# Performance work log

Measured on AMD Instinct MI355X. Metric: run time of the kernel, lower is better.

Reference implementation:

```python
import jax, jax.numpy as jnp
import numpy as np

B, N, C, H = 1, 128, 128, 8
D = C // H
SCALE = D ** -0.5


def layer_norm(x, w, b, eps=1e-5):
    m = jnp.mean(x, axis=-1, keepdims=True)
    v = jnp.var(x, axis=-1, keepdims=True)
    return (x - m) * jax.lax.rsqrt(v + eps) * w + b


def setup_inputs() -> dict:
    key = jax.random.key(0)
    ks = jax.random.split(key, 8)
    s = 0.02
    return {
        "e": jax.random.normal(ks[0], (B, N, N, C), jnp.float32),
        "mask": jnp.zeros((B, N, N, 1), jnp.float32),
        "ln_w": jnp.ones((C,), jnp.float32),
        "ln_b": jnp.zeros((C,), jnp.float32),
        "w_qkv_in": jax.random.normal(ks[1], (C, 3 * C), jnp.float32) * s,
        "b_qkv_in": jnp.zeros((3 * C,), jnp.float32),
        "w_eg_in": jax.random.normal(ks[2], (C, 2 * H), jnp.float32) * s,
        "b_eg_in": jnp.zeros((2 * H,), jnp.float32),
        "w_qkv_out": jax.random.normal(ks[3], (C, 3 * C), jnp.float32) * s,
        "b_qkv_out": jnp.zeros((3 * C,), jnp.float32),
        "w_eg_out": jax.random.normal(ks[4], (C, 2 * H), jnp.float32) * s,
        "b_eg_out": jnp.zeros((2 * H,), jnp.float32),
        "w_o": jax.random.normal(ks[5], (2 * C, C), jnp.float32) * s,
        "b_o": jnp.zeros((C,), jnp.float32),
    }


def reference(e, mask, ln_w, ln_b, w_qkv_in, b_qkv_in, w_eg_in, b_eg_in,
              w_qkv_out, b_qkv_out, w_eg_out, b_eg_out, w_o, b_o):
    b, n = e.shape[0], e.shape[1]
    e_ln = layer_norm(e, ln_w, ln_b)

    # ---- incoming-edge stream ----
    qkv = e_ln @ w_qkv_in + b_qkv_in                      # [b,n,n,3C]
    Q, K, V = jnp.split(qkv, 3, axis=-1)
    Q = Q.reshape(b, n, n, D, H) * SCALE                  # bijdh
    K = K.reshape(b, n, n, D, H)
    V = V.reshape(b, n, n, D, H)
    eg = e_ln @ w_eg_in + b_eg_in                         # [b,n,n,2H]
    E_in = eg[..., :H][:, :, None, :, :]                  # [b,i,1,k,h]
    G_in = eg[..., H:][:, :, None, :, :]
    H_in = jnp.einsum('bijdh,bjkdh->bijkh', Q, K) + E_in
    mask_in = mask[:, :, None, :, :]                      # [b,i,1,k,1]
    gates_in = jax.nn.sigmoid(G_in + mask_in)
    A_in = jax.nn.softmax(H_in + mask_in, axis=3) * gates_in
    Va_in = jnp.einsum('bijkh,bjkdh->bijdh', A_in, V)

    # ---- outgoing-edge stream ----
    qkv = e_ln @ w_qkv_out + b_qkv_out
    Q, K, V = jnp.split(qkv, 3, axis=-1)
    Q = Q.reshape(b, n, n, D, H) * SCALE
    K = K.reshape(b, n, n, D, H)
    V = V.reshape(b, n, n, D, H)
    eg = e_ln @ w_eg_out + b_eg_out
    E_out = eg[..., :H][:, :, :, None, :]                 # [b,k,i,1,h]
    G_out = eg[..., H:][:, :, :, None, :]
    H_out = jnp.einsum('bijdh,bkjdh->bkijh', Q, K) + E_out
    mask_out = mask[:, :, :, None, :]                     # [b,k,i,1,1]
    gates_out = jax.nn.sigmoid(G_out + mask_out)
    A_out = jax.nn.softmax(H_out + mask_out, axis=1) * gates_out
    Va_out = jnp.einsum('bkijh,bkjdh->bijdh', A_out, V)

    Va = jnp.concatenate([Va_in, Va_out], axis=-1).reshape(b, n, n, 2 * C)
    return Va @ w_o + b_o
```

## Files before the change

### kernel.cpp

```cpp
#include <hip/hip_runtime.h>
#include <hip/hip_bf16.h>


#define NPOS 16384
#define CDIM 128

typedef __attribute__((ext_vector_type(8))) short bf16x8;
typedef __attribute__((ext_vector_type(8))) unsigned short u16x8;
typedef __attribute__((ext_vector_type(4))) float f32x4;

#define MFMA16(a, b, c) __builtin_amdgcn_mfma_f32_16x16x32_bf16((a), (b), (c), 0, 0, 0)

#define GLL16(gp, lp) __builtin_amdgcn_global_load_lds( \
    (const __attribute__((address_space(1))) void*)(gp), \
    (__attribute__((address_space(3))) void*)(lp), 16, 0, 0)

static __device__ __forceinline__ unsigned short f2bf(float x) {
    union { float f; unsigned int u; } v; v.f = x;
    unsigned int u = v.u;
    unsigned int r = u + 0x7FFFu + ((u >> 16) & 1u);
    return (unsigned short)(r >> 16);
}
static __device__ __forceinline__ float bf2f(unsigned short h) {
    union { float f; unsigned int u; } v; v.u = ((unsigned int)h) << 16; return v.f;
}

__global__ __launch_bounds__(256) void ln_kernel(
    const float* __restrict__ e,
    const float* __restrict__ w,
    const float* __restrict__ b,
    unsigned short* __restrict__ e_hl)
{
    const int t = threadIdx.x;
    const int lane = t & 63;
    const int row = blockIdx.x * 4 + (t >> 6);
    float2 x = *(const float2*)(e + (size_t)row * CDIM + lane * 2);
    float s = x.x + x.y, s2 = x.x * x.x + x.y * x.y;
    #pragma unroll
    for (int off = 1; off < 64; off <<= 1) {
        s  += __shfl_xor(s,  off, 64);
        s2 += __shfl_xor(s2, off, 64);
    }
    float m = s * (1.f / 128.f);
    float v = s2 * (1.f / 128.f) - m * m;
    float sc = rsqrtf(v + 1e-5f);
    float2 wv = *(const float2*)(w + lane * 2);
    float2 bv = *(const float2*)(b + lane * 2);
    float y0 = (x.x - m) * sc * wv.x + bv.x;
    float y1 = (x.y - m) * sc * wv.y + bv.y;
    unsigned short h0 = f2bf(y0), h1 = f2bf(y1);
    ushort2 hi = {h0, h1};
    ushort2 lo = {f2bf(y0 - bf2f(h0)), f2bf(y1 - bf2f(h1))};
    *(ushort2*)(e_hl + (size_t)row * 256 + lane * 2)       = hi;
    *(ushort2*)(e_hl + (size_t)row * 256 + 128 + lane * 2) = lo;
}

__global__ __launch_bounds__(256) void pack_qkv_w(
    const float* __restrict__ wq, const float* __restrict__ we,
    unsigned short* __restrict__ Bt)
{
    int idx = blockIdx.x * 256 + threadIdx.x;
    int n = idx >> 7, k = idx & 127;
    float v = 0.f;
    if (n < 384) v = wq[(size_t)k * 384 + n];
    else if (n < 400) v = we[(size_t)k * 16 + (n - 384)];
    unsigned short hi = f2bf(v);
    Bt[idx] = hi;
    Bt[448 * 128 + idx] = f2bf(v - bf2f(hi));
}

__global__ __launch_bounds__(256) void pack_o_w(
    const float* __restrict__ wo, unsigned short* __restrict__ Bt)
{
    int idx = blockIdx.x * 256 + threadIdx.x;
    int n = idx >> 8, kp = idx & 255;
    int d = kp & 15, pl = kp >> 4;
    int k = d * 16 + pl;
    float v = wo[(size_t)k * 128 + n];
    unsigned short hi = f2bf(v);
    Bt[idx] = hi;
    Bt[128 * 256 + idx] = f2bf(v - bf2f(hi));
}

__global__ __launch_bounds__(256) void gemm_qkv_kernel(
    const unsigned short* __restrict__ e_hl,
    const unsigned short* __restrict__ B1t, const unsigned short* __restrict__ B2t,
    const float* __restrict__ bq_i, const float* __restrict__ be_i,
    const float* __restrict__ bq_o, const float* __restrict__ be_o,
    unsigned short* __restrict__ QT, unsigned short* __restrict__ KT,
    unsigned short* __restrict__ VT,
    float* __restrict__ eg_i, float* __restrict__ eg_o)
{
    __shared__ __align__(16) unsigned char smem[24576];
    unsigned short* Alds = (unsigned short*)smem;
    unsigned short* Blds = (unsigned short*)(smem + 16384);

    const int t = threadIdx.x;
    const int wave = t >> 6, lane = t & 63;
    const int m = lane & 15, q = lane >> 4;
    const int bx = blockIdx.x;
    const int W0blk = bx * 128;
    const int by = blockIdx.y;
    const int N0 = by * 64;
    const int br = blockIdx.z;
    const unsigned short* Bt = br ? B2t : B1t;
    const float* bias_qkv = br ? bq_o : bq_i;
    const float* bias_eg  = br ? be_o : be_i;
    float* eg = br ? eg_o : eg_i;

    f32x4 acc[2][4];
    #pragma unroll
    for (int a = 0; a < 2; ++a)
        #pragma unroll
        for (int c = 0; c < 4; ++c) acc[a][c] = (f32x4){0.f, 0.f, 0.f, 0.f};

    for (int kc = 0; kc < 4; ++kc) {
        #pragma unroll
        for (int ii = 0; ii < 6; ++ii) {
            const int id = wave + ii * 4;
            if (id < 16) {
                const int hl = id >> 3, s = id & 7;
                const int qq = s >> 1, rbase = (s & 1) * 64;
                const unsigned short* g = e_hl
                    + (size_t)(W0blk + rbase + lane) * 256 + hl * 128 + kc * 32 + qq * 8;
                unsigned short* l = Alds + hl * 4096 + qq * 1024 + rbase * 8;
                GLL16(g, l);
            } else {
                const int id2 = id - 16;
                const int hl = id2 >> 2, qq = id2 & 3;
                const unsigned short* g = Bt + (size_t)(N0 + lane) * 128
                    + hl * (448 * 128) + kc * 32 + qq * 8;
                unsigned short* l = Blds + hl * 2048 + qq * 512;
                GLL16(g, l);
            }
        }
        __syncthreads();

        bf16x8 aH[2], aL[2], bH[4], bL[4];
        #pragma unroll
        for (int ms = 0; ms < 2; ++ms) {
            const int row = wave * 32 + ms * 16 + m;
            aH[ms] = *(const bf16x8*)(Alds + 0    + q * 1024 + row * 8);
            aL[ms] = *(const bf16x8*)(Alds + 4096 + q * 1024 + row * 8);
        }
        #pragma unroll
        for (int ns = 0; ns < 4; ++ns) {
            bH[ns] = *(const bf16x8*)(Blds + 0    + q * 512 + (ns * 16 + m) * 8);
            bL[ns] = *(const bf16x8*)(Blds + 2048 + q * 512 + (ns * 16 + m) * 8);
        }
        #pragma unroll
        for (int ns = 0; ns < 4; ++ns) {
            acc[0][ns] = MFMA16(aH[0], bH[ns], acc[0][ns]);
            acc[1][ns] = MFMA16(aH[1], bH[ns], acc[1][ns]);
        }
        #pragma unroll
        for (int ns = 0; ns < 4; ++ns) {
            acc[0][ns] = MFMA16(aL[0], bH[ns], acc[0][ns]);
            acc[1][ns] = MFMA16(aL[1], bH[ns], acc[1][ns]);
        }
        #pragma unroll
        for (int ns = 0; ns < 4; ++ns) {
            acc[0][ns] = MFMA16(aH[0], bL[ns], acc[0][ns]);
            acc[1][ns] = MFMA16(aH[1], bL[ns], acc[1][ns]);
        }
        __syncthreads();
    }

    if (by < 6) {
        unsigned short (*Ts16)[66] = (unsigned short (*)[66])smem;
        #pragma unroll
        for (int ms = 0; ms < 2; ++ms)
            #pragma unroll
            for (int ns = 0; ns < 4; ++ns) {
                const int lc = ns * 16 + m;
                const int col = N0 + lc;
                const float bias = bias_qkv[col];
                const float scale = (col < 128) ? 0.25f : 1.f;
                #pragma unroll
                for (int r = 0; r < 4; ++r) {
                    const int lr = wave * 32 + ms * 16 + q * 4 + r;
                    Ts16[lr][lc] = f2bf((acc[ms][ns][r] + bias) * scale);
                }
            }
        __syncthreads();
        const int qsel = by >> 1, dhalf = by & 1;
        unsigned short* dstH = (qsel == 0) ? QT : (qsel == 1 ? KT : VT);
        #pragma unroll
        for (int it = 0; it < 4; ++it) {
            int item = it * 256 + t;
            int hh = item >> 7, lr = item & 127;
            u16x8 hi;
            #pragma unroll
            for (int dd = 0; dd < 8; ++dd)
                hi[dd] = Ts16[lr][dd * 8 + hh];
            size_t addr = (((size_t)(br * 8 + hh) * 2 + dhalf) * NPOS
                           + (size_t)bx * 128 + lr) * 8;
            *(u16x8*)(dstH + addr) = hi;
        }
    } else {
        float* Tf = (float*)smem;
        #pragma unroll
        for (int ms = 0; ms < 2; ++ms) {
            const float bias = bias_eg[m];
            #pragma unroll
            for (int r = 0; r < 4; ++r) {
                const int lr = wave * 32 + ms * 16 + q * 4 + r;
                Tf[lr * 33 + m] = acc[ms][0][r] + bias;
            }
        }
        __syncthreads();
        #pragma unroll
        for (int it = 0; it < 2; ++it) {
            const int g = it * 256 + t;
            const int r128 = g >> 2, q4 = g & 3;
            float4 val;
            val.x = Tf[r128 * 33 + q4 * 4 + 0];
            val.y = Tf[r128 * 33 + q4 * 4 + 1];
            val.z = Tf[r128 * 33 + q4 * 4 + 2];
            val.w = Tf[r128 * 33 + q4 * 4 + 3];
            *(float4*)(eg + (size_t)(bx * 128 + r128) * 16 + q4 * 4) = val;
        }
    }
}

__global__ __launch_bounds__(256) void transpose_kernel(
    unsigned short* __restrict__ QT, unsigned short* __restrict__ KT,
    unsigned short* __restrict__ VT)
{
    const int s = blockIdx.y;
    unsigned short* base;
    int sub;
    if (s < 32)       { base = QT; sub = s; }
    else if (s < 48)  { base = KT; sub = 16 + (s - 32); }
    else              { base = VT; sub = 16 + (s - 48); }
    unsigned short* P = base + (size_t)sub * NPOS * 8;

    int x = blockIdx.x, a = 0;
    while (x >= 8 - a) { x -= 8 - a; ++a; }
    const int b = a + x;

    __shared__ unsigned short T1[16][136];
    __shared__ unsigned short T2[16][136];

    const int t = threadIdx.x;
    const int r = t >> 4, c = t & 15;

    u16x8 v1 = *(const u16x8*)(P + ((size_t)(a * 16 + r) * 128 + b * 16 + c) * 8);
    *(u16x8*)&T1[r][c * 8] = v1;
    if (a != b) {
        u16x8 v2 = *(const u16x8*)(P + ((size_t)(b * 16 + r) * 128 + a * 16 + c) * 8);
        *(u16x8*)&T2[r][c * 8] = v2;
    }
    __syncthreads();

    u16x8 w1 = *(const u16x8*)&T1[c][r * 8];
    *(u16x8*)(P + ((size_t)(b * 16 + r) * 128 + a * 16 + c) * 8) = w1;
    if (a != b) {
        u16x8 w2 = *(const u16x8*)&T2[c][r * 8];
        *(u16x8*)(P + ((size_t)(a * 16 + r) * 128 + b * 16 + c) * 8) = w2;
    }
}

__global__ __launch_bounds__(256) void gemm_out_kernel(
    const float* __restrict__ va,
    const unsigned short* __restrict__ B3t,
    const float* __restrict__ bias,
    float* __restrict__ out)
{
    const int t = threadIdx.x;
    const int wave = t >> 6, lane = t & 63;
    const int m = lane & 15, q = lane >> 4;
    const int W0 = blockIdx.x * 64 + wave * 16;
    const int N0 = blockIdx.y * 64;

    f32x4 acc[4];
    #pragma unroll
    for (int c = 0; c < 4; ++c) acc[c] = (f32x4){0.f, 0.f, 0.f, 0.f};

    const float* arow = va + (size_t)(W0 + m) * 256;
    const unsigned short* bcol[4];
    #pragma unroll
    for (int ns = 0; ns < 4; ++ns)
        bcol[ns] = B3t + (size_t)(N0 + ns * 16 + m) * 256;

    #pragma unroll 2
    for (int kc = 0; kc < 8; ++kc) {
        const int ko = kc * 32 + q * 8;
        const float4* ap = (const float4*)(arow + ko);
        float4 f0 = ap[0], f1 = ap[1];
        float xs[8] = {f0.x, f0.y, f0.z, f0.w, f1.x, f1.y, f1.z, f1.w};
        bf16x8 ah, al;
        #pragma unroll
        for (int jj = 0; jj < 8; ++jj) {
            unsigned short h = f2bf(xs[jj]);
            ah[jj] = (short)h;
            al[jj] = (short)f2bf(xs[jj] - bf2f(h));
        }
        bf16x8 bh[4], bl[4];
        #pragma unroll
        for (int ns = 0; ns < 4; ++ns) {
            bh[ns] = *(const bf16x8*)(bcol[ns] + ko);
            bl[ns] = *(const bf16x8*)(bcol[ns] + 128 * 256 + ko);
        }
        #pragma unroll
        for (int ns = 0; ns < 4; ++ns) acc[ns] = MFMA16(ah, bh[ns], acc[ns]);
        #pragma unroll
        for (int ns = 0; ns < 4; ++ns) acc[ns] = MFMA16(al, bh[ns], acc[ns]);
        #pragma unroll
        for (int ns = 0; ns < 4; ++ns) acc[ns] = MFMA16(ah, bl[ns], acc[ns]);
    }

    #pragma unroll
    for (int ns = 0; ns < 4; ++ns) {
        const int col = N0 + ns * 16 + m;
        #pragma unroll
        for (int r = 0; r < 4; ++r) {
            const int prow = W0 + q * 4 + r;
            const int orow = ((prow & 127) << 7) | (prow >> 7);
            out[(size_t)orow * 128 + col] = acc[ns][r] + bias[col];
        }
    }
}

__global__ __launch_bounds__(256) void tables_kernel(
    const float* __restrict__ eg_in, const float* __restrict__ eg_out,
    const float* __restrict__ mask,
    float* __restrict__ Etab, float* __restrict__ Gtab)
{
    int flat = blockIdx.x * 256 + threadIdx.x;
    int br = flat >> 14;
    int p  = flat & 16383;
    const float* eg = br ? eg_out : eg_in;
    const float4* row = (const float4*)(eg + (size_t)p * 16);
    float4 r0 = row[0], r1 = row[1], r2 = row[2], r3 = row[3];
    float m = mask[p];
    float E[8] = {r0.x, r0.y, r0.z, r0.w, r1.x, r1.y, r1.z, r1.w};
    float G[8] = {r2.x, r2.y, r2.z, r2.w, r3.x, r3.y, r3.z, r3.w};
    int i, k;
    if (br == 0) { i = p >> 7; k = p & 127; }
    else         { k = p >> 7; i = p & 127; }
    int dst = i * 128 + k;
    #pragma unroll
    for (int h = 0; h < 8; ++h) {
        size_t off = (size_t)(br * 8 + h) * NPOS + dst;
        Etab[off] = E[h] + m;
        Gtab[off] = 1.f / (1.f + __expf(-(G[h] + m)));
    }
}

__global__ __launch_bounds__(256) void attn_kernel(
    const unsigned short* __restrict__ QT, const unsigned short* __restrict__ KT,
    const unsigned short* __restrict__ VT,
    const float* __restrict__ Etab, const float* __restrict__ Gtab,
    float* __restrict__ va)
{
    const int j = blockIdx.x, h = blockIdx.y, br = blockIdx.z;
    const int t = threadIdx.x;
    const int wave = t >> 6, lane = t & 63;
    const int m = lane & 15, q = lane >> 4;
    const int plane = br * 8 + h;
    const size_t SP = (size_t)NPOS * 8;
    const size_t jb = (size_t)j * 128 * 8;
    const float* __restrict__ Eb = Etab + (size_t)plane * NPOS;
    const float* __restrict__ Gb = Gtab + (size_t)plane * NPOS;

    __shared__ unsigned short Vth[16 * 136];
    __shared__ unsigned short Pl[128 * 136];

    const int strip = wave * 32;

    f32x4 S[2][8];
    #pragma unroll
    for (int mt = 0; mt < 2; ++mt)
        #pragma unroll
        for (int r = 0; r < 4; ++r) {
            const int i = strip + mt * 16 + q * 4 + r;
            const float* ep = Eb + (size_t)i * 128 + m * 8;
            f32x4 ea = *(const f32x4*)ep;
            f32x4 eb = *(const f32x4*)(ep + 4);
            #pragma unroll
            for (int nt = 0; nt < 4; ++nt) S[mt][nt][r]     = ea[nt];
            #pragma unroll
            for (int nt = 0; nt < 4; ++nt) S[mt][nt + 4][r] = eb[nt];
        }

    {
        int c = t >> 1, ch = t & 1;
        int krow = (c & 15) * 8 + (c >> 4);
        const unsigned short* src = VT + (size_t)(plane * 2 + ch) * SP + jb
                                  + (size_t)krow * 8;
        u16x8 v = *(const u16x8*)src;
        #pragma unroll
        for (int dd = 0; dd < 8; ++dd)
            Vth[(ch * 8 + dd) * 136 + c] = v[dd];
    }

    const bf16x8 zero8 = {};
    const int hf = q & 1;
    const size_t qko = (size_t)(plane * 2 + hf) * SP + jb;

    bf16x8 aQ[2];
    #pragma unroll
    for (int mt = 0; mt < 2; ++mt) {
        const size_t off = qko + (size_t)(strip + mt * 16 + m) * 8;
        aQ[mt] = (q < 2) ? *(const bf16x8*)(QT + off) : zero8;
    }

    #pragma unroll
    for (int nt = 0; nt < 8; ++nt) {
        const size_t koff = qko + (size_t)(m * 8 + nt) * 8;
        bf16x8 bK = (q < 2) ? *(const bf16x8*)(KT + koff) : zero8;
        #pragma unroll
        for (int mt = 0; mt < 2; ++mt)
            S[mt][nt] = MFMA16(aQ[mt], bK, S[mt][nt]);
    }

    #pragma unroll
    for (int mt = 0; mt < 2; ++mt)
        #pragma unroll
        for (int r = 0; r < 4; ++r) {
            float v = -1e30f;
            #pragma unroll
            for (int nt = 0; nt < 8; ++nt) v = fmaxf(v, S[mt][nt][r]);
            v = fmaxf(v, __shfl_xor(v, 1)); v = fmaxf(v, __shfl_xor(v, 2));
            v = fmaxf(v, __shfl_xor(v, 4)); v = fmaxf(v, __shfl_xor(v, 8));
            float s = 0.f;
            #pragma unroll
            for (int nt = 0; nt < 8; ++nt) {
                float p = __expf(S[mt][nt][r] - v);
                S[mt][nt][r] = p;
                s += p;
            }
            s += __shfl_xor(s, 1); s += __shfl_xor(s, 2);
            s += __shfl_xor(s, 4); s += __shfl_xor(s, 8);
            const float inv = 1.f / s;
            const int i = strip + mt * 16 + q * 4 + r;
            const float* gp = Gb + (size_t)i * 128 + m * 8;
            f32x4 ga = *(const f32x4*)gp;
            f32x4 gb = *(const f32x4*)(gp + 4);
            #pragma unroll
            for (int nt = 0; nt < 4; ++nt) {
                Pl[i * 136 + nt * 16 + m]       = f2bf(S[mt][nt][r] * inv * ga[nt]);
                Pl[i * 136 + (nt + 4) * 16 + m] = f2bf(S[mt][nt + 4][r] * inv * gb[nt]);
            }
        }

    __syncthreads();

    f32x4 av[2] = {(f32x4){0.f, 0.f, 0.f, 0.f}, (f32x4){0.f, 0.f, 0.f, 0.f}};
    #pragma unroll
    for (int kc = 0; kc < 4; ++kc) {
        const int off = kc * 32 + q * 8;
        bf16x8 bV = *(const bf16x8*)&Vth[m * 136 + off];
        #pragma unroll
        for (int mt = 0; mt < 2; ++mt) {
            bf16x8 aP = *(const bf16x8*)&Pl[(strip + mt * 16 + m) * 136 + off];
            av[mt] = MFMA16(aP, bV, av[mt]);
        }
    }

    #pragma unroll
    for (int mt = 0; mt < 2; ++mt)
        #pragma unroll
        for (int r = 0; r < 4; ++r) {
            const int i = strip + mt * 16 + q * 4 + r;
            va[((size_t)(j * 128 + i)) * 256 + plane * 16 + m] = av[mt][r];
        }
}

extern "C" void kernel_launch(void* const* d_in, const int* in_sizes, int n_in,
                              void* d_out, int out_size, void* d_ws, size_t ws_size,
                              hipStream_t stream) {
    const float* e        = (const float*)d_in[0];
    const float* mask     = (const float*)d_in[1];
    const float* ln_w     = (const float*)d_in[2];
    const float* ln_b     = (const float*)d_in[3];
    const float* w_qkv_in = (const float*)d_in[4];
    const float* b_qkv_in = (const float*)d_in[5];
    const float* w_eg_in  = (const float*)d_in[6];
    const float* b_eg_in  = (const float*)d_in[7];
    const float* w_qkv_o  = (const float*)d_in[8];
    const float* b_qkv_o  = (const float*)d_in[9];
    const float* w_eg_o   = (const float*)d_in[10];
    const float* b_eg_o   = (const float*)d_in[11];
    const float* w_o      = (const float*)d_in[12];
    const float* b_o      = (const float*)d_in[13];
    float* out = (float*)d_out;

    char* base = (char*)d_ws;
    const size_t PLANE = (size_t)16 * NPOS * 16;
    unsigned short* e_hl = (unsigned short*)base;
    unsigned short* QT = (unsigned short*)(base + (size_t)NPOS * 256 * 2);
    unsigned short* KT = QT + PLANE;
    unsigned short* VT = KT + PLANE;
    float* eg_i = (float*)(VT + PLANE);
    float* eg_o = eg_i + (size_t)NPOS * 16;
    float* va   = eg_o + (size_t)NPOS * 16;

    float* Etab = (float*)base;
    float* Gtab = Etab + (size_t)2 * 8 * NPOS;
    unsigned short* B3t = (unsigned short*)(base + 2 * 1024 * 1024 + 256 * 1024);
    unsigned short* B1t = (unsigned short*)va;
    unsigned short* B2t = B1t + (size_t)2 * 448 * 128;

    ln_kernel<<<NPOS / 4, 256, 0, stream>>>(e, ln_w, ln_b, e_hl);

    pack_qkv_w<<<224, 256, 0, stream>>>(w_qkv_in, w_eg_in, B1t);
    pack_qkv_w<<<224, 256, 0, stream>>>(w_qkv_o,  w_eg_o,  B2t);

    gemm_qkv_kernel<<<dim3(128, 7, 2), 256, 0, stream>>>(
        e_hl, B1t, B2t, b_qkv_in, b_eg_in, b_qkv_o, b_eg_o,
        QT, KT, VT, eg_i, eg_o);

    transpose_kernel<<<dim3(36, 64), 256, 0, stream>>>(QT, KT, VT);

    pack_o_w<<<128, 256, 0, stream>>>(w_o, B3t);

    tables_kernel<<<128, 256, 0, stream>>>(eg_i, eg_o, mask, Etab, Gtab);

    attn_kernel<<<dim3(128, 8, 2), 256, 0, stream>>>(
        QT, KT, VT, Etab, Gtab, va);

    gemm_out_kernel<<<dim3(256, 2), 256, 0, stream>>>(va, B3t, b_o, out);
}
```

Before: 186.4 us.

## Fuse prep kernels, compute E/G tables in QKV GEMM epilogue, store as bf16

Merges the layernorm and three weight-packing launches into one prep kernel. The tables kernel is removed: the QKV GEMM epilogue adds the mask, applies the sigmoid and writes the E and G tables directly, transposed for the outgoing branch. The tables are now stored in bf16, so attention reads half the bytes. This cuts launch overhead and an intermediate round trip, at the cost of bf16 precision on the edge bias and gate values.

Measured after the change: 172.6 us. 1.08x faster.

```diff
diff --git a/kernel.cpp b/kernel.cpp
--- a/kernel.cpp
+++ b/kernel.cpp
@@ -25,61 +25,62 @@
     union { float f; unsigned int u; } v; v.u = ((unsigned int)h) << 16; return v.f;
 }
 
-__global__ __launch_bounds__(256) void ln_kernel(
-    const float* __restrict__ e,
-    const float* __restrict__ w,
-    const float* __restrict__ b,
-    unsigned short* __restrict__ e_hl)
+__global__ __launch_bounds__(256) void prep_kernel(
+    const float* __restrict__ e, const float* __restrict__ lnw,
+    const float* __restrict__ lnb, unsigned short* __restrict__ e_hl,
+    const float* __restrict__ wq1, const float* __restrict__ we1,
+    unsigned short* __restrict__ B1t,
+    const float* __restrict__ wq2, const float* __restrict__ we2,
+    unsigned short* __restrict__ B2t,
+    const float* __restrict__ wo, unsigned short* __restrict__ B3t)
 {
     const int t = threadIdx.x;
-    const int lane = t & 63;
-    const int row = blockIdx.x * 4 + (t >> 6);
-    float2 x = *(const float2*)(e + (size_t)row * CDIM + lane * 2);
-    float s = x.x + x.y, s2 = x.x * x.x + x.y * x.y;
-    #pragma unroll
-    for (int off = 1; off < 64; off <<= 1) {
-        s  += __shfl_xor(s,  off, 64);
-        s2 += __shfl_xor(s2, off, 64);
-    }
-    float m = s * (1.f / 128.f);
-    float v = s2 * (1.f / 128.f) - m * m;
-    float sc = rsqrtf(v + 1e-5f);
-    float2 wv = *(const float2*)(w + lane * 2);
-    float2 bv = *(const float2*)(b + lane * 2);
-    float y0 = (x.x - m) * sc * wv.x + bv.x;
-    float y1 = (x.y - m) * sc * wv.y + bv.y;
-    unsigned short h0 = f2bf(y0), h1 = f2bf(y1);
-    ushort2 hi = {h0, h1};
-    ushort2 lo = {f2bf(y0 - bf2f(h0)), f2bf(y1 - bf2f(h1))};
-    *(ushort2*)(e_hl + (size_t)row * 256 + lane * 2)       = hi;
-    *(ushort2*)(e_hl + (size_t)row * 256 + 128 + lane * 2) = lo;
-}
-
-__global__ __launch_bounds__(256) void pack_qkv_w(
-    const float* __restrict__ wq, const float* __restrict__ we,
-    unsigned short* __restrict__ Bt)
-{
-    int idx = blockIdx.x * 256 + threadIdx.x;
-    int n = idx >> 7, k = idx & 127;
-    float v = 0.f;
-    if (n < 384) v = wq[(size_t)k * 384 + n];
-    else if (n < 400) v = we[(size_t)k * 16 + (n - 384)];
-    unsigned short hi = f2bf(v);
-    Bt[idx] = hi;
-    Bt[448 * 128 + idx] = f2bf(v - bf2f(hi));
-}
-
-__global__ __launch_bounds__(256) void pack_o_w(
-    const float* __restrict__ wo, unsigned short* __restrict__ Bt)
-{
-    int idx = blockIdx.x * 256 + threadIdx.x;
-    int n = idx >> 8, kp = idx & 255;
-    int d = kp & 15, pl = kp >> 4;
-    int k = d * 16 + pl;
-    float v = wo[(size_t)k * 128 + n];
-    unsigned short hi = f2bf(v);
-    Bt[idx] = hi;
-    Bt[128 * 256 + idx] = f2bf(v - bf2f(hi));
+    const int bx = blockIdx.x;
+    if (bx < 4096) {
+        const int lane = t & 63;
+        const int row = bx * 4 + (t >> 6);
+        float2 x = *(const float2*)(e + (size_t)row * CDIM + lane * 2);
+        float s = x.x + x.y, s2 = x.x * x.x + x.y * x.y;
+        #pragma unroll
+        for (int off = 1; off < 64; off <<= 1) {
+            s  += __shfl_xor(s,  off, 64);
+            s2 += __shfl_xor(s2, off, 64);
+        }
+        float m = s * (1.f / 128.f);
+        float v = s2 * (1.f / 128.f) - m * m;
+        float sc = rsqrtf(v + 1e-5f);
+        float2 wv = *(const float2*)(lnw + lane * 2);
+        float2 bv = *(const float2*)(lnb + lane * 2);
+        float y0 = (x.x - m) * sc * wv.x + bv.x;
+        float y1 = (x.y - m) * sc * wv.y + bv.y;
+        unsigned short h0 = f2bf(y0), h1 = f2bf(y1);
+        ushort2 hi = {h0, h1};
+        ushort2 lo = {f2bf(y0 - bf2f(h0)), f2bf(y1 - bf2f(h1))};
+        *(ushort2*)(e_hl + (size_t)row * 256 + lane * 2)       = hi;
+        *(ushort2*)(e_hl + (size_t)row * 256 + 128 + lane * 2) = lo;
+    } else if (bx < 4544) {
+        int pb = bx - 4096;
+        const float* wq; const float* we; unsigned short* Bt;
+        if (pb < 224) { wq = wq1; we = we1; Bt = B1t; }
+        else          { pb -= 224; wq = wq2; we = we2; Bt = B2t; }
+        const int idx = pb * 256 + t;
+        const int n = idx >> 7, k = idx & 127;
+        float v = 0.f;
+        if (n < 384) v = wq[(size_t)k * 384 + n];
+        else if (n < 400) v = we[(size_t)k * 16 + (n - 384)];
+        unsigned short hi = f2bf(v);
+        Bt[idx] = hi;
+        Bt[448 * 128 + idx] = f2bf(v - bf2f(hi));
+    } else {
+        const int idx = (bx - 4544) * 256 + t;
+        const int n = idx >> 8, kp = idx & 255;
+        const int d = kp & 15, pl = kp >> 4;
+        const int k = d * 16 + pl;
+        float v = wo[(size_t)k * 128 + n];
+        unsigned short hi = f2bf(v);
+        B3t[idx] = hi;
+        B3t[128 * 256 + idx] = f2bf(v - bf2f(hi));
+    }
 }
 
 __global__ __launch_bounds__(256) void gemm_qkv_kernel(
@@ -87,9 +88,10 @@
     const unsigned short* __restrict__ B1t, const unsigned short* __restrict__ B2t,
     const float* __restrict__ bq_i, const float* __restrict__ be_i,
     const float* __restrict__ bq_o, const float* __restrict__ be_o,
+    const float* __restrict__ mask,
     unsigned short* __restrict__ QT, unsigned short* __restrict__ KT,
     unsigned short* __restrict__ VT,
-    float* __restrict__ eg_i, float* __restrict__ eg_o)
+    unsigned short* __restrict__ Etab, unsigned short* __restrict__ Gtab)
 {
     __shared__ __align__(16) unsigned char smem[24576];
     unsigned short* Alds = (unsigned short*)smem;
@@ -106,7 +108,6 @@
     const unsigned short* Bt = br ? B2t : B1t;
     const float* bias_qkv = br ? bq_o : bq_i;
     const float* bias_eg  = br ? be_o : be_i;
-    float* eg = br ? eg_o : eg_i;
 
     f32x4 acc[2][4];
     #pragma unroll
@@ -209,16 +210,21 @@
             }
         }
         __syncthreads();
-        #pragma unroll
-        for (int it = 0; it < 2; ++it) {
-            const int g = it * 256 + t;
-            const int r128 = g >> 2, q4 = g & 3;
-            float4 val;
-            val.x = Tf[r128 * 33 + q4 * 4 + 0];
-            val.y = Tf[r128 * 33 + q4 * 4 + 1];
-            val.z = Tf[r128 * 33 + q4 * 4 + 2];
-            val.w = Tf[r128 * 33 + q4 * 4 + 3];
-            *(float4*)(eg + (size_t)(bx * 128 + r128) * 16 + q4 * 4) = val;
+        const int r128 = t & 127, grp = t >> 7;
+        const float mk = mask[bx * 128 + r128];
+        const int dst = br ? (r128 * 128 + bx) : (bx * 128 + r128);
+        if (grp == 0) {
+            #pragma unroll
+            for (int h = 0; h < 8; ++h)
+                Etab[(size_t)(br * 8 + h) * NPOS + dst] =
+                    f2bf(Tf[r128 * 33 + h] + mk);
+        } else {
+            #pragma unroll
+            for (int h = 0; h < 8; ++h) {
+                const float g = Tf[r128 * 33 + 8 + h] + mk;
+                Gtab[(size_t)(br * 8 + h) * NPOS + dst] =
+                    f2bf(1.f / (1.f + __expf(-g)));
+            }
         }
     }
 }
@@ -322,36 +328,10 @@
     }
 }
 
-__global__ __launch_bounds__(256) void tables_kernel(
-    const float* __restrict__ eg_in, const float* __restrict__ eg_out,
-    const float* __restrict__ mask,
-    float* __restrict__ Etab, float* __restrict__ Gtab)
-{
-    int flat = blockIdx.x * 256 + threadIdx.x;
-    int br = flat >> 14;
-    int p  = flat & 16383;
-    const float* eg = br ? eg_out : eg_in;
-    const float4* row = (const float4*)(eg + (size_t)p * 16);
-    float4 r0 = row[0], r1 = row[1], r2 = row[2], r3 = row[3];
-    float m = mask[p];
-    float E[8] = {r0.x, r0.y, r0.z, r0.w, r1.x, r1.y, r1.z, r1.w};
-    float G[8] = {r2.x, r2.y, r2.z, r2.w, r3.x, r3.y, r3.z, r3.w};
-    int i, k;
-    if (br == 0) { i = p >> 7; k = p & 127; }
-    else         { k = p >> 7; i = p & 127; }
-    int dst = i * 128 + k;
-    #pragma unroll
-    for (int h = 0; h < 8; ++h) {
-        size_t off = (size_t)(br * 8 + h) * NPOS + dst;
-        Etab[off] = E[h] + m;
-        Gtab[off] = 1.f / (1.f + __expf(-(G[h] + m)));
-    }
-}
-
 __global__ __launch_bounds__(256) void attn_kernel(
     const unsigned short* __restrict__ QT, const unsigned short* __restrict__ KT,
     const unsigned short* __restrict__ VT,
-    const float* __restrict__ Etab, const float* __restrict__ Gtab,
+    const unsigned short* __restrict__ Etab, const unsigned short* __restrict__ Gtab,
     float* __restrict__ va)
 {
     const int j = blockIdx.x, h = blockIdx.y, br = blockIdx.z;
@@ -361,8 +341,8 @@
     const int plane = br * 8 + h;
     const size_t SP = (size_t)NPOS * 8;
     const size_t jb = (size_t)j * 128 * 8;
-    const float* __restrict__ Eb = Etab + (size_t)plane * NPOS;
-    const float* __restrict__ Gb = Gtab + (size_t)plane * NPOS;
+    const unsigned short* __restrict__ Eb = Etab + (size_t)plane * NPOS;
+    const unsigned short* __restrict__ Gb = Gtab + (size_t)plane * NPOS;
 
     __shared__ unsigned short Vth[16 * 136];
     __shared__ unsigned short Pl[128 * 136];
@@ -375,13 +355,9 @@
         #pragma unroll
         for (int r = 0; r < 4; ++r) {
             const int i = strip + mt * 16 + q * 4 + r;
-            const float* ep = Eb + (size_t)i * 128 + m * 8;
-            f32x4 ea = *(const f32x4*)ep;
-            f32x4 eb = *(const f32x4*)(ep + 4);
-            #pragma unroll
-            for (int nt = 0; nt < 4; ++nt) S[mt][nt][r]     = ea[nt];
-            #pragma unroll
-            for (int nt = 0; nt < 4; ++nt) S[mt][nt + 4][r] = eb[nt];
+            u16x8 ev = *(const u16x8*)(Eb + (size_t)i * 128 + m * 8);
+            #pragma unroll
+            for (int nt = 0; nt < 8; ++nt) S[mt][nt][r] = bf2f(ev[nt]);
         }
 
     {
@@ -435,13 +411,13 @@
             s += __shfl_xor(s, 4); s += __shfl_xor(s, 8);
             const float inv = 1.f / s;
             const int i = strip + mt * 16 + q * 4 + r;
-            const float* gp = Gb + (size_t)i * 128 + m * 8;
-            f32x4 ga = *(const f32x4*)gp;
-            f32x4 gb = *(const f32x4*)(gp + 4);
+            u16x8 gv = *(const u16x8*)(Gb + (size_t)i * 128 + m * 8);
             #pragma unroll
             for (int nt = 0; nt < 4; ++nt) {
-                Pl[i * 136 + nt * 16 + m]       = f2bf(S[mt][nt][r] * inv * ga[nt]);
-                Pl[i * 136 + (nt + 4) * 16 + m] = f2bf(S[mt][nt + 4][r] * inv * gb[nt]);
+                Pl[i * 136 + nt * 16 + m] =
+                    f2bf(S[mt][nt][r] * inv * bf2f(gv[nt]));
+                Pl[i * 136 + (nt + 4) * 16 + m] =
+                    f2bf(S[mt][nt + 4][r] * inv * bf2f(gv[nt + 4]));
             }
         }
 
@@ -493,30 +469,23 @@
     unsigned short* QT = (unsigned short*)(base + (size_t)NPOS * 256 * 2);
     unsigned short* KT = QT + PLANE;
     unsigned short* VT = KT + PLANE;
-    float* eg_i = (float*)(VT + PLANE);
-    float* eg_o = eg_i + (size_t)NPOS * 16;
-    float* va   = eg_o + (size_t)NPOS * 16;
-
-    float* Etab = (float*)base;
-    float* Gtab = Etab + (size_t)2 * 8 * NPOS;
-    unsigned short* B3t = (unsigned short*)(base + 2 * 1024 * 1024 + 256 * 1024);
+    float* va = (float*)(VT + PLANE);
+    unsigned short* Etab = (unsigned short*)(va + (size_t)NPOS * 256);
+    unsigned short* Gtab = Etab + (size_t)16 * NPOS;
+    unsigned short* B3t  = Gtab + (size_t)16 * NPOS;
+
     unsigned short* B1t = (unsigned short*)va;
     unsigned short* B2t = B1t + (size_t)2 * 448 * 128;
 
-    ln_kernel<<<NPOS / 4, 256, 0, stream>>>(e, ln_w, ln_b, e_hl);
-
-    pack_qkv_w<<<224, 256, 0, stream>>>(w_qkv_in, w_eg_in, B1t);
-    pack_qkv_w<<<224, 256, 0, stream>>>(w_qkv_o,  w_eg_o,  B2t);
+    prep_kernel<<<4672, 256, 0, stream>>>(
+        e, ln_w, ln_b, e_hl,
+        w_qkv_in, w_eg_in, B1t, w_qkv_o, w_eg_o, B2t, w_o, B3t);
 
     gemm_qkv_kernel<<<dim3(128, 7, 2), 256, 0, stream>>>(
-        e_hl, B1t, B2t, b_qkv_in, b_eg_in, b_qkv_o, b_eg_o,
-        QT, KT, VT, eg_i, eg_o);
+        e_hl, B1t, B2t, b_qkv_in, b_eg_in, b_qkv_o, b_eg_o, mask,
+        QT, KT, VT, Etab, Gtab);
 
     transpose_kernel<<<dim3(36, 64), 256, 0, stream>>>(QT, KT, VT);
-
-    pack_o_w<<<128, 256, 0, stream>>>(w_o, B3t);
-
-    tables_kernel<<<128, 256, 0, stream>>>(eg_i, eg_o, mask, Etab, Gtab);
 
     attn_kernel<<<dim3(128, 8, 2), 256, 0, stream>>>(
         QT, KT, VT, Etab, Gtab, va);
```
